# Performance work log

Measured on AMD Instinct MI355X. Metric: run time of the kernel, lower is better.

The kernel has to match this reference:

```python
import jax, jax.numpy as jnp
import numpy as np

N_ATOMS = 100000
N_BONDS = 200000
MAX_NB = 6
ATOM_FDIM = 133
BOND_FDIM = 147
HIDDEN = 300
DEPTH = 3
N_MOLS = 4000


def setup_inputs() -> dict:
    key = jax.random.key(0)
    ks = jax.random.split(key, 10)
    f_atoms = jax.random.normal(ks[0], (N_ATOMS, ATOM_FDIM), dtype=jnp.float32)
    f_bonds = jax.random.normal(ks[1], (N_BONDS, BOND_FDIM), dtype=jnp.float32)
    a2b = jax.random.randint(ks[2], (N_ATOMS, MAX_NB), 0, N_BONDS, dtype=jnp.int32)
    b2a = jax.random.randint(ks[3], (N_BONDS,), 0, N_ATOMS, dtype=jnp.int32)
    b2revb = jax.random.randint(ks[4], (N_BONDS,), 0, N_BONDS, dtype=jnp.int32)
    mol_ids = jnp.sort(jax.random.randint(ks[5], (N_ATOMS,), 0, N_MOLS, dtype=jnp.int32))
    # learned params (W_i, W_h have bias=False; W_o has bias)
    sc = 0.02
    W_i = jax.random.normal(ks[6], (BOND_FDIM, HIDDEN), dtype=jnp.float32) * sc
    W_h = jax.random.normal(ks[7], (HIDDEN, HIDDEN), dtype=jnp.float32) * sc
    W_o = jax.random.normal(ks[8], (ATOM_FDIM + HIDDEN, HIDDEN), dtype=jnp.float32) * sc
    b_o = jax.random.normal(ks[9], (HIDDEN,), dtype=jnp.float32) * sc
    return {"f_atoms": f_atoms, "f_bonds": f_bonds, "a2b": a2b, "b2a": b2a,
            "b2revb": b2revb, "mol_ids": mol_ids, "W_i": W_i, "W_h": W_h,
            "W_o": W_o, "b_o": b_o}


def reference(f_atoms, f_bonds, a2b, b2a, b2revb, mol_ids, W_i, W_h, W_o, b_o):
    # input = W_i(f_bonds); message = relu(input)
    inp = f_bonds @ W_i                              # [n_bonds, H]
    message = jax.nn.relu(inp)
    for _ in range(DEPTH - 1):
        # gather incoming-bond messages per atom and sum over neighbors
        a_message = message[a2b].sum(axis=1)         # [n_atoms, H]
        # directed-bond update: m_b = sum_in(src atom) - reverse message
        message = a_message[b2a] - message[b2revb]   # [n_bonds, H]
        message = jax.nn.relu(inp + message @ W_h)   # dropout p=0 -> identity
    a_message = message[a2b].sum(axis=1)             # [n_atoms, H]
    a_input = jnp.concatenate([f_atoms, a_message], axis=1)
    atom_hiddens = jax.nn.relu(a_input @ W_o + b_o)  # [n_atoms, H]
    # per-molecule mean aggregation (a_scope loop -> segment ops)
    sums = jax.ops.segment_sum(atom_hiddens, mol_ids, num_segments=N_MOLS)
    counts = jax.ops.segment_sum(jnp.ones((atom_hiddens.shape[0], 1), atom_hiddens.dtype),
                                 mol_ids, num_segments=N_MOLS)
    # empty molecules -> cached zero vector
    return jnp.where(counts > 0, sums / jnp.maximum(counts, 1.0), 0.0)
```

## Files before the change

### kernel.cpp

```cpp
#include <hip/hip_runtime.h>

typedef unsigned short bfraw;
typedef __attribute__((ext_vector_type(8))) short short8v;
typedef __attribute__((ext_vector_type(8))) unsigned short ushort8v;
typedef __attribute__((ext_vector_type(4))) float f32x4;

static __device__ __forceinline__ float bf2f(unsigned short u) {
    union { unsigned int i; float f; } c; c.i = ((unsigned int)u) << 16; return c.f;
}
static __device__ __forceinline__ unsigned short f2bf(float f) {
    union { float f; unsigned int i; } c; c.f = f;
    unsigned int r = c.i + 0x7fffu + ((c.i >> 16) & 1u);
    return (unsigned short)(r >> 16);
}
static __device__ __forceinline__ unsigned short brelu(unsigned short u) {
    return (u & 0x8000u) ? (unsigned short)0 : u;
}
static __device__ __forceinline__ f32x4 mfma16(short8v a, short8v b, f32x4 c) {
    return __builtin_amdgcn_mfma_f32_16x16x32_bf16(a, b, c, 0, 0, 0);
}

__global__ __launch_bounds__(64) void k_pack(const float* __restrict__ W, int Krows, int row_off,
                                             bfraw* __restrict__ out) {
    const int b = blockIdx.x;
    const int ks = b / 20, ct = b - ks * 20;
    const int l = threadIdx.x;
    const int n = ct * 16 + (l & 15);
    const int kb = ks * 32 + (l >> 4) * 8;
    short8v pk;
#pragma unroll
    for (int j = 0; j < 8; ++j) {
        int k = kb + j;
        float v = (k < Krows && n < 300) ? W[(row_off + k) * 300 + n] : 0.f;
        pk[j] = (short)f2bf(v);
    }
    *(short8v*)&out[(b * 64 + l) * 8] = pk;
}


__global__ __launch_bounds__(512, 4) void k_in(const float* __restrict__ fb,
                                               const bfraw* __restrict__ Wp,
                                               bfraw* __restrict__ inp) {
    __shared__ short A[64 * 40 * 8];
    const int row0 = blockIdx.x * 64;
    const int tid = threadIdx.x;
    if (tid < 128) {
        int r = tid >> 1, c = 18 + (tid & 1);
        short8v z = {0, 0, 0, 0, 0, 0, 0, 0};
        *(short8v*)&A[(r * 40 + (c ^ (r & 7))) * 8] = z;
    }
    __syncthreads();
    const float4* fb4 = (const float4*)(fb + (long long)row0 * 147);
#pragma unroll 1
    for (int s = 0; s < 5; ++s) {
        int idx = tid + s * 512;
        if (idx < 2352) {
            float4 v = fb4[idx];
            const float* ve = (const float*)&v;
            int k0 = idx * 4;
#pragma unroll
            for (int e = 0; e < 4; ++e) {
                int k = k0 + e;
                int r = k / 147;
                int c = k - r * 147;
                A[(r * 40 + ((c >> 3) ^ (r & 7))) * 8 + (c & 7)] = (short)f2bf(ve[e]);
            }
        }
    }
    __syncthreads();
    const int w = tid >> 6, l = tid & 63;
    const int wr = w >> 2, wc = w & 3;
    const int lr = l & 15, lk = l >> 4, sw = l & 7;
    f32x4 acc[2][5];
#pragma unroll
    for (int ri = 0; ri < 2; ++ri)
#pragma unroll
        for (int i = 0; i < 5; ++i) acc[ri][i] = (f32x4){0.f, 0.f, 0.f, 0.f};
    const short8v* Ald = (const short8v*)A;
#pragma unroll
    for (int ks = 0; ks < 5; ++ks) {
        short8v bfr[2], wv[5];
#pragma unroll
        for (int ri = 0; ri < 2; ++ri)
            bfr[ri] = Ald[((wr * 2 + ri) * 16 + lr) * 40 + ((ks * 4 + lk) ^ sw)];
#pragma unroll
        for (int i = 0; i < 5; ++i)
            wv[i] = *(const short8v*)&Wp[((ks * 20 + wc * 5 + i) * 64 + l) * 8];
#pragma unroll
        for (int ri = 0; ri < 2; ++ri)
#pragma unroll
            for (int i = 0; i < 5; ++i)
                acc[ri][i] = mfma16(wv[i], bfr[ri], acc[ri][i]);
    }
    __syncthreads();
#pragma unroll
    for (int ri = 0; ri < 2; ++ri)
#pragma unroll
        for (int i = 0; i < 5; ++i) {
            const int r = (wr * 2 + ri) * 16 + lr;
            const int c16 = (wc * 5 + i) * 2 + (lk >> 1);
            ushort4 t;
            t.x = f2bf(acc[ri][i][0]); t.y = f2bf(acc[ri][i][1]);
            t.z = f2bf(acc[ri][i][2]); t.w = f2bf(acc[ri][i][3]);
            *(ushort4*)&A[(r * 40 + (c16 ^ (r & 7))) * 8 + (lk & 1) * 4] = t;
        }
    __syncthreads();
    for (int idx = tid; idx < 64 * 38; idx += 512) {
        int r = idx / 38, c = idx - r * 38;
        short8v t = *(const short8v*)&A[(r * 40 + (c ^ (r & 7))) * 8];
        *(short8v*)&inp[(long long)(row0 + r) * 304 + c * 8] = t;
    }
}

__global__ __launch_bounds__(256) void k_gather(const bfraw* __restrict__ msg,
                                                const int* __restrict__ a2b,
                                                bfraw* __restrict__ amsg) {
    int gid = blockIdx.x * 256 + threadIdx.x;
    if (gid >= 100000 * 19) return;
    int a = gid / 19, c = gid - a * 19;
    const int* nb = a2b + a * 6;
    float s0[8], s1[8];
#pragma unroll
    for (int e = 0; e < 8; ++e) { s0[e] = 0.f; s1[e] = 0.f; }
#pragma unroll
    for (int j = 0; j < 6; ++j) {
        const long long base = (long long)nb[j] * 304;
        const ushort8v v0 = *(const ushort8v*)&msg[base + c * 8];
        const ushort8v v1 = *(const ushort8v*)&msg[base + (c + 19) * 8];
#pragma unroll
        for (int e = 0; e < 8; ++e) {
            s0[e] += bf2f(brelu(v0[e]));
            s1[e] += bf2f(brelu(v1[e]));
        }
    }
    short8v o0, o1;
#pragma unroll
    for (int e = 0; e < 8; ++e) { o0[e] = (short)f2bf(s0[e]); o1[e] = (short)f2bf(s1[e]); }
    *(short8v*)&amsg[(long long)a * 304 + c * 8] = o0;
    *(short8v*)&amsg[(long long)a * 304 + (c + 19) * 8] = o1;
}

__global__ __launch_bounds__(512, 4) void k_bond(const bfraw* __restrict__ amsg,
                                                 const bfraw* __restrict__ msg,
                                                 const bfraw* __restrict__ inp,
                                                 const int* __restrict__ b2a,
                                                 const int* __restrict__ b2revb,
                                                 const bfraw* __restrict__ Wp,
                                                 bfraw* __restrict__ out) {
    __shared__ short A[64 * 40 * 8];
    const int row0 = blockIdx.x * 64;
    const int tid = threadIdx.x;
    if (tid < 128) {
        int r = tid >> 1, c = 38 + (tid & 1);
        short8v z = {0, 0, 0, 0, 0, 0, 0, 0};
        *(short8v*)&A[(r * 40 + (c ^ (r & 7))) * 8] = z;
    }
    int rr[5], cc[5], ia[5], irv[5];
#pragma unroll
    for (int s = 0; s < 5; ++s) {
        int idx = tid + s * 512;
        if (s < 4 || idx < 2432) {
            rr[s] = idx / 38; cc[s] = idx - rr[s] * 38;
            const int b = row0 + rr[s];
            ia[s] = b2a[b];
            irv[s] = b2revb[b];
        }
    }
    ushort8v va[5], vm[5];
#pragma unroll
    for (int s = 0; s < 5; ++s) {
        int idx = tid + s * 512;
        if (s < 4 || idx < 2432) {
            va[s] = *(const ushort8v*)&amsg[(long long)ia[s] * 304 + cc[s] * 8];
            vm[s] = *(const ushort8v*)&msg[(long long)irv[s] * 304 + cc[s] * 8];
        }
    }
#pragma unroll
    for (int s = 0; s < 5; ++s) {
        int idx = tid + s * 512;
        if (s < 4 || idx < 2432) {
            short8v pk;
#pragma unroll
            for (int j = 0; j < 8; ++j)
                pk[j] = (short)f2bf(bf2f(va[s][j]) - bf2f(brelu(vm[s][j])));
            *(short8v*)&A[(rr[s] * 40 + (cc[s] ^ (rr[s] & 7))) * 8] = pk;
        }
    }
    __syncthreads();
    const int w = tid >> 6, l = tid & 63;
    const int wr = w >> 2, wc = w & 3;
    const int lr = l & 15, lk = l >> 4, sw = l & 7;
    f32x4 acc[2][5];
#pragma unroll
    for (int ri = 0; ri < 2; ++ri)
#pragma unroll
        for (int i = 0; i < 5; ++i) acc[ri][i] = (f32x4){0.f, 0.f, 0.f, 0.f};
    const short8v* Ald = (const short8v*)A;
#pragma unroll
    for (int ks = 0; ks < 10; ++ks) {
        short8v bfr[2], wv[5];
#pragma unroll
        for (int ri = 0; ri < 2; ++ri)
            bfr[ri] = Ald[((wr * 2 + ri) * 16 + lr) * 40 + ((ks * 4 + lk) ^ sw)];
#pragma unroll
        for (int i = 0; i < 5; ++i)
            wv[i] = *(const short8v*)&Wp[((ks * 20 + wc * 5 + i) * 64 + l) * 8];
#pragma unroll
        for (int ri = 0; ri < 2; ++ri)
#pragma unroll
            for (int i = 0; i < 5; ++i)
                acc[ri][i] = mfma16(wv[i], bfr[ri], acc[ri][i]);
    }
    __syncthreads();
#pragma unroll
    for (int ri = 0; ri < 2; ++ri)
#pragma unroll
        for (int i = 0; i < 5; ++i) {
            const int r = (wr * 2 + ri) * 16 + lr;
            const int c16 = (wc * 5 + i) * 2 + (lk >> 1);
            ushort4 t;
            t.x = f2bf(acc[ri][i][0]); t.y = f2bf(acc[ri][i][1]);
            t.z = f2bf(acc[ri][i][2]); t.w = f2bf(acc[ri][i][3]);
            *(ushort4*)&A[(r * 40 + (c16 ^ (r & 7))) * 8 + (lk & 1) * 4] = t;
        }
    __syncthreads();
    ushort8v ip[5];
#pragma unroll
    for (int s = 0; s < 5; ++s) {
        int idx = tid + s * 512;
        if (s < 4 || idx < 2432) {
            int r = idx / 38, c = idx - r * 38;
            ip[s] = *(const ushort8v*)&inp[(long long)(row0 + r) * 304 + c * 8];
        }
    }
#pragma unroll
    for (int s = 0; s < 5; ++s) {
        int idx = tid + s * 512;
        if (s < 4 || idx < 2432) {
            int r = idx / 38, c = idx - r * 38;
            short8v t = *(const short8v*)&A[(r * 40 + (c ^ (r & 7))) * 8];
            short8v m;
#pragma unroll
            for (int j = 0; j < 8; ++j)
                m[j] = (short)f2bf(bf2f(ip[s][j]) + bf2f((unsigned short)t[j]));
            *(short8v*)&out[(long long)(row0 + r) * 304 + c * 8] = m;
        }
    }
}

__global__ __launch_bounds__(512, 4) void k_out(const float* __restrict__ fa,
                                                const bfraw* __restrict__ msg,
                                                const int* __restrict__ a2b,
                                                const bfraw* __restrict__ WfP,
                                                const bfraw* __restrict__ WaP,
                                                const float* __restrict__ bo,
                                                bfraw* __restrict__ hid) {
    __shared__ short A[64 * 40 * 8];
    const int row0 = blockIdx.x * 64;
    const int tid = threadIdx.x;
    const int nvalid = (row0 + 64 <= 100000) ? 64 : (100000 - row0);
#pragma unroll
    for (int it = 0; it < 5; ++it) {
        int idx = tid + it * 512;
        int r = idx / 40, c = idx - r * 40;
        const int row = row0 + r;
        short8v pk;
        if (c < 38 && row < 100000) {
            const int* nb = a2b + row * 6;
            float s[8];
#pragma unroll
            for (int e = 0; e < 8; ++e) s[e] = 0.f;
#pragma unroll
            for (int j = 0; j < 6; ++j) {
                const ushort8v v = *(const ushort8v*)&msg[(long long)nb[j] * 304 + c * 8];
#pragma unroll
                for (int e = 0; e < 8; ++e) s[e] += bf2f(brelu(v[e]));
            }
#pragma unroll
            for (int e = 0; e < 8; ++e) pk[e] = (short)f2bf(s[e]);
        } else {
#pragma unroll
            for (int j = 0; j < 8; ++j) pk[j] = 0;
        }
        *(short8v*)&A[(r * 40 + (c ^ (r & 7))) * 8] = pk;
    }
    __syncthreads();
    const int w = tid >> 6, l = tid & 63;
    const int wr = w >> 2, wc = w & 3;
    const int lr = l & 15, lk = l >> 4, sw = l & 7;
    f32x4 acc[2][5];
#pragma unroll
    for (int ri = 0; ri < 2; ++ri)
#pragma unroll
        for (int i = 0; i < 5; ++i) acc[ri][i] = (f32x4){0.f, 0.f, 0.f, 0.f};
    const short8v* Ald = (const short8v*)A;
#pragma unroll
    for (int ks = 0; ks < 10; ++ks) {
        short8v bfr[2], wv[5];
#pragma unroll
        for (int ri = 0; ri < 2; ++ri)
            bfr[ri] = Ald[((wr * 2 + ri) * 16 + lr) * 40 + ((ks * 4 + lk) ^ sw)];
#pragma unroll
        for (int i = 0; i < 5; ++i)
            wv[i] = *(const short8v*)&WaP[((ks * 20 + wc * 5 + i) * 64 + l) * 8];
#pragma unroll
        for (int ri = 0; ri < 2; ++ri)
#pragma unroll
            for (int i = 0; i < 5; ++i)
                acc[ri][i] = mfma16(wv[i], bfr[ri], acc[ri][i]);
    }
    __syncthreads();
    if (tid < 256) {
        int r = tid >> 2, c = 16 + (tid & 3);
        short8v z = {0, 0, 0, 0, 0, 0, 0, 0};
        *(short8v*)&A[(r * 40 + (c ^ (r & 7))) * 8] = z;
    }
    __syncthreads();
    {
        const float4* fa4 = (const float4*)(fa + (long long)row0 * 133);
        const int limit4 = (nvalid * 133) >> 2;
#pragma unroll 1
        for (int s = 0; s < 5; ++s) {
            int idx = tid + s * 512;
            if (idx < limit4) {
                float4 v = fa4[idx];
                const float* ve = (const float*)&v;
                int k0 = idx * 4;
#pragma unroll
                for (int e = 0; e < 4; ++e) {
                    int k = k0 + e;
                    int r = k / 133;
                    int c = k - r * 133;
                    A[(r * 40 + ((c >> 3) ^ (r & 7))) * 8 + (c & 7)] = (short)f2bf(ve[e]);
                }
            }
        }
    }
    __syncthreads();
#pragma unroll
    for (int ks = 0; ks < 5; ++ks) {
        short8v bfr[2], wv[5];
#pragma unroll
        for (int ri = 0; ri < 2; ++ri)
            bfr[ri] = Ald[((wr * 2 + ri) * 16 + lr) * 40 + ((ks * 4 + lk) ^ sw)];
#pragma unroll
        for (int i = 0; i < 5; ++i)
            wv[i] = *(const short8v*)&WfP[((ks * 20 + wc * 5 + i) * 64 + l) * 8];
#pragma unroll
        for (int ri = 0; ri < 2; ++ri)
#pragma unroll
            for (int i = 0; i < 5; ++i)
                acc[ri][i] = mfma16(wv[i], bfr[ri], acc[ri][i]);
    }
    __syncthreads();
#pragma unroll
    for (int ri = 0; ri < 2; ++ri)
#pragma unroll
        for (int i = 0; i < 5; ++i) {
            const int r = (wr * 2 + ri) * 16 + lr;
            const int c16 = (wc * 5 + i) * 2 + (lk >> 1);
            ushort4 t;
            t.x = f2bf(acc[ri][i][0]); t.y = f2bf(acc[ri][i][1]);
            t.z = f2bf(acc[ri][i][2]); t.w = f2bf(acc[ri][i][3]);
            *(ushort4*)&A[(r * 40 + (c16 ^ (r & 7))) * 8 + (lk & 1) * 4] = t;
        }
    __syncthreads();
    for (int idx = tid; idx < 64 * 38; idx += 512) {
        int r = idx / 38, c = idx - r * 38;
        const int row = row0 + r;
        if (row >= 100000) continue;
        short8v t = *(const short8v*)&A[(r * 40 + (c ^ (r & 7))) * 8];
        float4 b0 = *(const float4*)&bo[c * 8];
        float4 b1 = (c < 37) ? *(const float4*)&bo[c * 8 + 4]
                             : make_float4(0.f, 0.f, 0.f, 0.f);
        float bias[8] = {b0.x, b0.y, b0.z, b0.w, b1.x, b1.y, b1.z, b1.w};
        short8v m;
#pragma unroll
        for (int j = 0; j < 8; ++j)
            m[j] = (short)f2bf(fmaxf(bf2f((unsigned short)t[j]) + bias[j], 0.f));
        *(short8v*)&hid[(long long)row * 304 + c * 8] = m;
    }
}

__global__ __launch_bounds__(320) void k_mean(const bfraw* __restrict__ hid,
                                              const int* __restrict__ mol,
                                              float* __restrict__ out) {
    __shared__ float red[8][304];
    const int m = blockIdx.x;
    const int natoms = 100000;
    int lo = 0, hi = natoms;
    while (lo < hi) { int mid = (lo + hi) >> 1; if (mol[mid] < m) lo = mid + 1; else hi = mid; }
    const int start = lo;
    lo = start; hi = natoms;
    while (lo < hi) { int mid = (lo + hi) >> 1; if (mol[mid] <= m) lo = mid + 1; else hi = mid; }
    const int end = lo;
    const int tid = threadIdx.x;
    const int p = tid / 38, c = tid - p * 38;
    if (tid < 304) {
        float s[8];
#pragma unroll
        for (int e = 0; e < 8; ++e) s[e] = 0.f;
        for (int a = start + p; a < end; a += 8) {
            const ushort8v v = *(const ushort8v*)&hid[(long long)a * 304 + c * 8];
#pragma unroll
            for (int e = 0; e < 8; ++e) s[e] += bf2f(v[e]);
        }
#pragma unroll
        for (int e = 0; e < 8; ++e) red[p][c * 8 + e] = s[e];
    }
    __syncthreads();
    if (tid < 300) {
        float t = 0.f;
#pragma unroll
        for (int p2 = 0; p2 < 8; ++p2) t += red[p2][tid];
        const int n = end - start;
        out[m * 300 + tid] = (n > 0) ? (t / (float)n) : 0.f;
    }
}

extern "C" void kernel_launch(void* const* d_in, const int* in_sizes, int n_in,
                              void* d_out, int out_size, void* d_ws, size_t ws_size,
                              hipStream_t stream) {
    const float* f_atoms = (const float*)d_in[0];
    const float* f_bonds = (const float*)d_in[1];
    const int* a2b      = (const int*)d_in[2];
    const int* b2a      = (const int*)d_in[3];
    const int* b2revb   = (const int*)d_in[4];
    const int* mol_ids  = (const int*)d_in[5];
    const float* W_i    = (const float*)d_in[6];
    const float* W_h    = (const float*)d_in[7];
    const float* W_o    = (const float*)d_in[8];
    const float* b_o    = (const float*)d_in[9];
    float* out = (float*)d_out;

    char* wsb = (char*)d_ws;
    bfraw* inp  = (bfraw*)(wsb);
    bfraw* M1   = (bfraw*)(wsb + 121600000ll);
    bfraw* M2   = (bfraw*)(wsb + 243200000ll);
    bfraw* amsg = (bfraw*)(wsb + 364800000ll);
    bfraw* WiP   = (bfraw*)(wsb + 425600000ll);
    bfraw* WhP   = (bfraw*)(wsb + 425702400ll);
    bfraw* WoFaP = (bfraw*)(wsb + 425907200ll);
    bfraw* WoAmP = (bfraw*)(wsb + 426009600ll);

    k_pack<<<100, 64, 0, stream>>>(W_i, 147, 0, WiP);
    k_pack<<<200, 64, 0, stream>>>(W_h, 300, 0, WhP);
    k_pack<<<100, 64, 0, stream>>>(W_o, 133, 0, WoFaP);
    k_pack<<<200, 64, 0, stream>>>(W_o, 300, 133, WoAmP);

    const int nb_blocks = 200000 / 64;
    const int na_blocks = (100000 + 63) / 64;
    const int gather_blocks = (100000 * 19 + 255) / 256;

    k_in<<<nb_blocks, 512, 0, stream>>>(f_bonds, WiP, inp);

    k_gather<<<gather_blocks, 256, 0, stream>>>(inp, a2b, amsg);
    k_bond<<<nb_blocks, 512, 0, stream>>>(amsg, inp, inp, b2a, b2revb, WhP, M1);
    k_gather<<<gather_blocks, 256, 0, stream>>>(M1, a2b, amsg);
    k_bond<<<nb_blocks, 512, 0, stream>>>(amsg, M1, inp, b2a, b2revb, WhP, M2);

    bfraw* hid = M1;
    k_out<<<na_blocks, 512, 0, stream>>>(f_atoms, M2, a2b, WoFaP, WoAmP, b_o, hid);
    k_mean<<<4000, 320, 0, stream>>>(hid, mol_ids, out);
}
```

Measured before the change: 603.3 us.

## Fuse per-molecule segment sum into output kernel with atomics; batch neighbor gathers

The output kernel now reduces relu(hidden+bias) per molecule directly from shared memory and atomically adds partial sums into the output, so the bf16 hidden tensor is never written and re-read. A light normalization kernel then divides by the atom counts, and the output is zeroed with a memset first. The a2b neighbor gather is also restructured to issue loads for two slices before accumulating, to raise memory-level parallelism. This adds float atomic contention and order-dependent rounding, and holds more vector registers at once.

```diff
diff --git a/kernel.cpp b/kernel.cpp
--- a/kernel.cpp
+++ b/kernel.cpp
@@ -254,35 +254,55 @@
                                                 const bfraw* __restrict__ WfP,
                                                 const bfraw* __restrict__ WaP,
                                                 const float* __restrict__ bo,
-                                                bfraw* __restrict__ hid) {
+                                                const int* __restrict__ mol,
+                                                float* __restrict__ outp) {
     __shared__ short A[64 * 40 * 8];
     const int row0 = blockIdx.x * 64;
     const int tid = threadIdx.x;
     const int nvalid = (row0 + 64 <= 100000) ? 64 : (100000 - row0);
-#pragma unroll
-    for (int it = 0; it < 5; ++it) {
-        int idx = tid + it * 512;
-        int r = idx / 40, c = idx - r * 40;
-        const int row = row0 + r;
-        short8v pk;
-        if (c < 38 && row < 100000) {
-            const int* nb = a2b + row * 6;
-            float s[8];
-#pragma unroll
-            for (int e = 0; e < 8; ++e) s[e] = 0.f;
-#pragma unroll
-            for (int j = 0; j < 6; ++j) {
-                const ushort8v v = *(const ushort8v*)&msg[(long long)nb[j] * 304 + c * 8];
-#pragma unroll
-                for (int e = 0; e < 8; ++e) s[e] += bf2f(brelu(v[e]));
+#pragma unroll 1
+    for (int sp = 0; sp < 5; sp += 2) {
+        ushort8v v[2][6];
+        int ur[2], uc[2], act[2];
+#pragma unroll
+        for (int u = 0; u < 2; ++u) {
+            act[u] = 0;
+            int s = sp + u;
+            if (s < 5) {
+                int idx = tid + s * 512;
+                int r = idx / 40, c = idx - r * 40;
+                ur[u] = r; uc[u] = c;
+                const int row = row0 + r;
+                if (c < 38 && row < 100000) {
+                    act[u] = 1;
+                    const int* nb = a2b + row * 6;
+#pragma unroll
+                    for (int j = 0; j < 6; ++j)
+                        v[u][j] = *(const ushort8v*)&msg[(long long)nb[j] * 304 + c * 8];
+                }
             }
-#pragma unroll
-            for (int e = 0; e < 8; ++e) pk[e] = (short)f2bf(s[e]);
-        } else {
-#pragma unroll
-            for (int j = 0; j < 8; ++j) pk[j] = 0;
-        }
-        *(short8v*)&A[(r * 40 + (c ^ (r & 7))) * 8] = pk;
+        }
+#pragma unroll
+        for (int u = 0; u < 2; ++u) {
+            int s = sp + u;
+            if (s >= 5) continue;
+            short8v pk;
+            if (act[u]) {
+                float sm[8];
+#pragma unroll
+                for (int e = 0; e < 8; ++e) sm[e] = 0.f;
+#pragma unroll
+                for (int j = 0; j < 6; ++j)
+#pragma unroll
+                    for (int e = 0; e < 8; ++e) sm[e] += bf2f(brelu(v[u][j][e]));
+#pragma unroll
+                for (int e = 0; e < 8; ++e) pk[e] = (short)f2bf(sm[e]);
+            } else {
+#pragma unroll
+                for (int e = 0; e < 8; ++e) pk[e] = 0;
+            }
+            *(short8v*)&A[(ur[u] * 40 + (uc[u] ^ (ur[u] & 7))) * 8] = pk;
+        }
     }
     __syncthreads();
     const int w = tid >> 6, l = tid & 63;
@@ -365,27 +385,32 @@
             *(ushort4*)&A[(r * 40 + (c16 ^ (r & 7))) * 8 + (lk & 1) * 4] = t;
         }
     __syncthreads();
-    for (int idx = tid; idx < 64 * 38; idx += 512) {
-        int r = idx / 38, c = idx - r * 38;
-        const int row = row0 + r;
-        if (row >= 100000) continue;
-        short8v t = *(const short8v*)&A[(r * 40 + (c ^ (r & 7))) * 8];
-        float4 b0 = *(const float4*)&bo[c * 8];
-        float4 b1 = (c < 37) ? *(const float4*)&bo[c * 8 + 4]
-                             : make_float4(0.f, 0.f, 0.f, 0.f);
-        float bias[8] = {b0.x, b0.y, b0.z, b0.w, b1.x, b1.y, b1.z, b1.w};
-        short8v m;
-#pragma unroll
-        for (int j = 0; j < 8; ++j)
-            m[j] = (short)f2bf(fmaxf(bf2f((unsigned short)t[j]) + bias[j], 0.f));
-        *(short8v*)&hid[(long long)row * 304 + c * 8] = m;
-    }
-}
-
-__global__ __launch_bounds__(320) void k_mean(const bfraw* __restrict__ hid,
-                                              const int* __restrict__ mol,
+    if (tid < 300) {
+        const int j = tid;
+        const float bj = bo[j];
+        float s = 0.f;
+        int cur = -1;
+        const int st = tid & 63;
+        for (int k = 0; k < 64; ++k) {
+            const int r = (st + k) & 63;
+            if (r < nvalid) {
+                const int mo = mol[row0 + r];
+                float vv = bf2f((unsigned short)A[(r * 40 + ((j >> 3) ^ (r & 7))) * 8 + (j & 7)]);
+                vv = fmaxf(vv + bj, 0.f);
+                if (mo != cur) {
+                    if (cur >= 0 && s != 0.f) atomicAdd(&outp[cur * 300 + j], s);
+                    cur = mo; s = vv;
+                } else {
+                    s += vv;
+                }
+            }
+        }
+        if (cur >= 0 && s != 0.f) atomicAdd(&outp[cur * 300 + j], s);
+    }
+}
+
+__global__ __launch_bounds__(320) void k_norm(const int* __restrict__ mol,
                                               float* __restrict__ out) {
-    __shared__ float red[8][304];
     const int m = blockIdx.x;
     const int natoms = 100000;
     int lo = 0, hi = natoms;
@@ -393,28 +418,11 @@
     const int start = lo;
     lo = start; hi = natoms;
     while (lo < hi) { int mid = (lo + hi) >> 1; if (mol[mid] <= m) lo = mid + 1; else hi = mid; }
-    const int end = lo;
+    const int n = lo - start;
     const int tid = threadIdx.x;
-    const int p = tid / 38, c = tid - p * 38;
-    if (tid < 304) {
-        float s[8];
-#pragma unroll
-        for (int e = 0; e < 8; ++e) s[e] = 0.f;
-        for (int a = start + p; a < end; a += 8) {
-            const ushort8v v = *(const ushort8v*)&hid[(long long)a * 304 + c * 8];
-#pragma unroll
-            for (int e = 0; e < 8; ++e) s[e] += bf2f(v[e]);
-        }
-#pragma unroll
-        for (int e = 0; e < 8; ++e) red[p][c * 8 + e] = s[e];
-    }
-    __syncthreads();
     if (tid < 300) {
-        float t = 0.f;
-#pragma unroll
-        for (int p2 = 0; p2 < 8; ++p2) t += red[p2][tid];
-        const int n = end - start;
-        out[m * 300 + tid] = (n > 0) ? (t / (float)n) : 0.f;
+        float v = out[m * 300 + tid];
+        out[m * 300 + tid] = (n > 0) ? (v / (float)n) : 0.f;
     }
 }
 
@@ -443,6 +451,8 @@
     bfraw* WoFaP = (bfraw*)(wsb + 425907200ll);
     bfraw* WoAmP = (bfraw*)(wsb + 426009600ll);
 
+    hipMemsetAsync(out, 0, (size_t)out_size * sizeof(float), stream);
+
     k_pack<<<100, 64, 0, stream>>>(W_i, 147, 0, WiP);
     k_pack<<<200, 64, 0, stream>>>(W_h, 300, 0, WhP);
     k_pack<<<100, 64, 0, stream>>>(W_o, 133, 0, WoFaP);
@@ -459,7 +469,7 @@
     k_gather<<<gather_blocks, 256, 0, stream>>>(M1, a2b, amsg);
     k_bond<<<nb_blocks, 512, 0, stream>>>(amsg, M1, inp, b2a, b2revb, WhP, M2);
 
-    bfraw* hid = M1;
-    k_out<<<na_blocks, 512, 0, stream>>>(f_atoms, M2, a2b, WoFaP, WoAmP, b_o, hid);
-    k_mean<<<4000, 320, 0, stream>>>(hid, mol_ids, out);
-}
+    k_out<<<na_blocks, 512, 0, stream>>>(f_atoms, M2, a2b, WoFaP, WoAmP, b_o,
+                                         mol_ids, out);
+    k_norm<<<4000, 320, 0, stream>>>(mol_ids, out);
+}
```

Result: slower. 702.6 us (+16.5%).
